# Kernel optimization log

Measured on AMD Instinct MI355X. Metric: run time of the kernel, lower is better.

The kernel has to match this reference:

```python
import jax, jax.numpy as jnp
import numpy as np

# Bit-slice configuration from the module defaults: slices [1,1,2,4] -> 8-bit signed INT.
# The crossbar engine's MapReduceDot decomposes the quantized integers into bit-planes,
# runs partial dot products per (input-slice, weight-slice) pair across paral_size
# partitions, and recombines them with 2^shift weights. In the ideal (noise-free)
# engine this recombination is EXACT, so the forward math equals:
#   dequant(blockwise_quant(x)) @ dequant(blockwise_quant(W^T)) + bias
# with per-block scales determined by the quant granularities.
IN_BITS = 1 + 1 + 2 + 4   # sum(input_slice)  = 8
W_BITS = 1 + 1 + 2 + 4    # sum(weight_slice) = 8
IN_GRAN = (1, 32)         # (rows, cols) blocks over (seq, in_features)
W_GRAN = (32, 32)         # blocks over (in_features, out_features) of weight.t()


def block_fake_quant(x, bits, gran):
    """Symmetric per-block fake quantization (quantize -> dequantize).

    x: [..., R, C]; gran=(gr, gc) tiles the last two dims. Each (gr, gc) block
    gets its own max-abs scale, matching SlicedData's quant_gran semantics.
    """
    qmax = float(2 ** (bits - 1) - 1)  # 127 for 8-bit
    gr, gc = gran
    lead = x.shape[:-2]
    R, C = x.shape[-2], x.shape[-1]
    xb = x.reshape(*lead, R // gr, gr, C // gc, gc)
    mx = jnp.max(jnp.abs(xb), axis=(-3, -1), keepdims=True)
    scale = jnp.where(mx > 0, mx / qmax, jnp.ones_like(mx))
    q = jnp.clip(jnp.round(xb / scale), -qmax, qmax) * scale
    return q.reshape(x.shape)


def setup_inputs() -> dict:
    key = jax.random.key(0)
    k1, k2, k3 = jax.random.split(key, 3)
    B, S, Din, Dout = 4, 4096, 2048, 2048
    x = jax.random.normal(k1, (B, S, Din), dtype=jnp.float32)
    # kaiming_uniform_(a=sqrt(5)) on a Linear weight is U(-1/sqrt(fan_in), 1/sqrt(fan_in))
    bound = 1.0 / np.sqrt(Din)
    weight = jax.random.uniform(k2, (Dout, Din), jnp.float32, -bound, bound)
    bias = jax.random.uniform(k3, (Dout,), jnp.float32, -bound, bound)
    return {"x": x, "weight": weight, "bias": bias}


def reference(x, weight, bias):
    # Quantize activations per (1, 32) block and weight.t() per (32, 32) block,
    # then recombine via the (mathematically exact) bit-sliced dot == dense GEMM
    # on the dequantized values.
    qx = block_fake_quant(x, IN_BITS, IN_GRAN)            # [B, S, Din]
    qw = block_fake_quant(weight.T, W_BITS, W_GRAN)       # [Din, Dout]
    out = jnp.einsum('bsd,de->bse', qx, qw) + bias        # [B, S, Dout]
    return out
```

## Files before the change

kernel.cpp:

```cpp
#include <hip/hip_runtime.h>
#include <hip/hip_bf16.h>
#include <stdint.h>

#define M_TOT 16384
#define N_TOT 2048
#define K_TOT 2048
#define NT 32

typedef __attribute__((ext_vector_type(8))) short bf16x8;
typedef __attribute__((ext_vector_type(4))) float f32x4;

__device__ __forceinline__ ushort f32_to_bf16_rne(float f) {
    uint32_t u = __float_as_uint(f);
    uint32_t r = (u + 0x7fffu + ((u >> 16) & 1u)) >> 16;
    return (ushort)r;
}

__device__ __forceinline__ void async_copy16(const void* gptr, void* lptr) {
    __builtin_amdgcn_global_load_lds(
        (const __attribute__((address_space(1))) uint32_t*)gptr,
        (__attribute__((address_space(3))) uint32_t*)lptr,
        16, 0, 0);
}

__global__ void quant_x_kernel(const float* __restrict__ x, ushort* __restrict__ qx) {
    const int tid = blockIdx.x * 256 + threadIdx.x;
    const float4 v = ((const float4*)x)[tid];
    float m = fmaxf(fmaxf(fabsf(v.x), fabsf(v.y)), fmaxf(fabsf(v.z), fabsf(v.w)));
    m = fmaxf(m, __shfl_xor(m, 1));
    m = fmaxf(m, __shfl_xor(m, 2));
    m = fmaxf(m, __shfl_xor(m, 4));
    const float s = (m > 0.f) ? (m / 127.f) : 1.f;
    const float q0 = fminf(fmaxf(rintf(v.x / s), -127.f), 127.f) * s;
    const float q1 = fminf(fmaxf(rintf(v.y / s), -127.f), 127.f) * s;
    const float q2 = fminf(fmaxf(rintf(v.z / s), -127.f), 127.f) * s;
    const float q3 = fminf(fmaxf(rintf(v.w / s), -127.f), 127.f) * s;
    ushort4 r;
    r.x = f32_to_bf16_rne(q0);
    r.y = f32_to_bf16_rne(q1);
    r.z = f32_to_bf16_rne(q2);
    r.w = f32_to_bf16_rne(q3);
    ((ushort4*)qx)[tid] = r;
}

__global__ void quant_w_kernel(const float* __restrict__ w, ushort* __restrict__ qw) {
    const int gtid = blockIdx.x * 256 + threadIdx.x;
    const int wid  = gtid >> 6;
    const int lane = gtid & 63;
    const int tn = wid >> 6;
    const int tk = wid & 63;
    const int row = tn * 32 + (lane >> 1);
    const int col = tk * 32 + ((lane & 1) << 4);
    const float* p = w + (size_t)row * K_TOT + col;
    const float4 v0 = ((const float4*)p)[0];
    const float4 v1 = ((const float4*)p)[1];
    const float4 v2 = ((const float4*)p)[2];
    const float4 v3 = ((const float4*)p)[3];
    float m = 0.f;
#define MAX4(V) m = fmaxf(m, fmaxf(fmaxf(fabsf(V.x), fabsf(V.y)), fmaxf(fabsf(V.z), fabsf(V.w))));
    MAX4(v0) MAX4(v1) MAX4(v2) MAX4(v3)
#undef MAX4
    #pragma unroll
    for (int off = 1; off < 64; off <<= 1) m = fmaxf(m, __shfl_xor(m, off));
    const float s = (m > 0.f) ? (m / 127.f) : 1.f;
    float vv[16] = {v0.x, v0.y, v0.z, v0.w, v1.x, v1.y, v1.z, v1.w,
                    v2.x, v2.y, v2.z, v2.w, v3.x, v3.y, v3.z, v3.w};
    union { ushort us[16]; uint4 q[2]; } o;
    #pragma unroll
    for (int i = 0; i < 16; ++i) {
        const float q = fminf(fmaxf(rintf(vv[i] / s), -127.f), 127.f) * s;
        o.us[i] = f32_to_bf16_rne(q);
    }
    uint4* dst = (uint4*)(qw + (size_t)row * K_TOT + col);
    dst[0] = o.q[0];
    dst[1] = o.q[1];
}

#define LDSA(tb, row, colus) \
    (*(const bf16x8*)&As[tb][row][(colus) ^ (((row) & 7) << 3)])
#define LDSB(slot, row, colus) \
    (*(const bf16x8*)&Bs[slot][row][(colus) ^ (((row) & 7) << 3)])

#define STAGE_A(tb, hh, li, tt)                                                          \
    async_copy16(Agbase + (size_t)((hh) * 128 + (li) * 64) * K_TOT + (size_t)(tt) * 64,  \
                 (char*)&As[0][0][0] + (tb) * 32768 + (hh) * 16384 + (li) * 8192 + (wv << 10));
#define STAGE_B(slot, hh, li, tt)                                                        \
    async_copy16(Bgbase + (size_t)((hh) * 128 + (li) * 64) * K_TOT + (size_t)(tt) * 64,  \
                 (char*)&Bs[0][0][0] + (size_t)(slot) * 32768 + (hh) * 16384 + (li) * 8192 + (wv << 10));
#define STAGE_A2(tb, hh, tt)    { STAGE_A(tb, hh, 0, tt) STAGE_A(tb, hh, 1, tt) }
#define STAGE_B2(slot, hh, tt)  { STAGE_B(slot, hh, 0, tt) STAGE_B(slot, hh, 1, tt) }

#define WAITLGKM4 { asm volatile("s_waitcnt lgkmcnt(4)" ::: "memory"); __builtin_amdgcn_sched_barrier(0); }
#define WAITLGKM0 { asm volatile("s_waitcnt lgkmcnt(0)" ::: "memory"); __builtin_amdgcn_sched_barrier(0); }

#define RD_AF(DST, tb, q) {                                   \
    DST[0] = LDSA(tb, ab + (q) * 32,      h8);                \
    DST[1] = LDSA(tb, ab + (q) * 32,      32 + h8);           \
    DST[2] = LDSA(tb, ab + (q) * 32 + 16, h8);                \
    DST[3] = LDSA(tb, ab + (q) * 32 + 16, 32 + h8); }

#define RD_BG(slot) {                                                         \
    _Pragma("unroll")                                                         \
    for (int j = 0; j < 4; ++j) {                                             \
        const int bb = wcn * 64 + j * 16 + r;                                 \
        bg[j][0] = LDSB(slot, bb, h8);  bg[j][1] = LDSB(slot, bb, 32 + h8);   \
    } }

#define MFMA_PH(i0, AF)                                                                   \
    __builtin_amdgcn_s_setprio(1);                                                        \
    _Pragma("unroll")                                                                     \
    for (int j = 0; j < 4; ++j) {                                                         \
        acc[i0][j]     = __builtin_amdgcn_mfma_f32_16x16x32_bf16(AF[0], bg[j][0], acc[i0][j], 0, 0, 0);     \
        acc[i0][j]     = __builtin_amdgcn_mfma_f32_16x16x32_bf16(AF[1], bg[j][1], acc[i0][j], 0, 0, 0);     \
        acc[(i0)+1][j] = __builtin_amdgcn_mfma_f32_16x16x32_bf16(AF[2], bg[j][0], acc[(i0)+1][j], 0, 0, 0); \
        acc[(i0)+1][j] = __builtin_amdgcn_mfma_f32_16x16x32_bf16(AF[3], bg[j][1], acc[(i0)+1][j], 0, 0, 0); \
    }                                                                                     \
    __builtin_amdgcn_s_setprio(0);

#define TILE_BODY(tb, t, STA, STB, VMC, BRD, BWR)                                         \
  {                                                                                       \
                   \
    RD_AF(afX, tb, 0)                                                                     \
    RD_BG(BRD)                                                                            \
    RD_AF(afY, tb, 1)                                                                     \
    if (STA) STAGE_A2(tb ^ 1, 0, (t) + 1)                                                 \
    WAITLGKM4                                                                             \
    MFMA_PH(0, afX)                                                                       \
                                        \
    RD_AF(afX, tb, 2)                                                                     \
    if (STA) STAGE_A2(tb ^ 1, 1, (t) + 1)                                                 \
    WAITLGKM4                                                                             \
    MFMA_PH(2, afY)                                                                       \
                     \
    RD_AF(afY, tb, 3)                                                                     \
    if (STB) STAGE_B2(BWR, 0, (t) + 2)                                                    \
    WAITLGKM4                                                                             \
    MFMA_PH(4, afX)                                                                       \
                    \
    if (STB) STAGE_B2(BWR, 1, (t) + 2)                                                    \
    WAITLGKM0                                                                             \
    MFMA_PH(6, afY)                                                                       \
    if ((VMC) == 4)      { asm volatile("s_waitcnt vmcnt(4)" ::: "memory"); }             \
    else if ((VMC) == 0) { asm volatile("s_waitcnt vmcnt(0)" ::: "memory"); }             \
    __builtin_amdgcn_s_barrier();          \
  }

__global__ __launch_bounds__(512, 2) void gemm_pipe5_kernel(
    const ushort* __restrict__ A,
    const ushort* __restrict__ Bt,
    const float* __restrict__ bias,
    float* __restrict__ C) {

    __shared__ ushort As[2][256][64];
    __shared__ ushort Bs[3][256][64];

    const int tid  = threadIdx.x;
    const int lane = tid & 63;
    const int wv   = tid >> 6;
    const int wmr  = wv >> 2;
    const int wcn  = wv & 3;
    const int r    = lane & 15;
    const int h8   = (lane >> 4) << 3;

    const int nbn  = N_TOT / 256;
    const int nwg  = (M_TOT / 256) * nbn;
    const int cpx  = nwg >> 3;
    const int swz  = (blockIdx.x & 7) * cpx + (blockIdx.x >> 3);
    const int brow = (swz / nbn) * 256;
    const int bcol = (swz % nbn) * 256;

    const int srow = tid >> 3;
    const int scol = (((tid & 7) ^ (srow & 7)) << 3);
    const ushort* Agbase = A  + (size_t)(brow + srow) * K_TOT + scol;
    const ushort* Bgbase = Bt + (size_t)(bcol + srow) * K_TOT + scol;

    const int ab = wmr * 128 + r;

    f32x4 acc[8][4];
    const f32x4 zero = {0.f, 0.f, 0.f, 0.f};
    #pragma unroll
    for (int i = 0; i < 8; ++i)
        #pragma unroll
        for (int j = 0; j < 4; ++j) acc[i][j] = zero;

    STAGE_A2(0, 0, 0) STAGE_A2(0, 1, 0)
    STAGE_B2(0, 0, 0) STAGE_B2(0, 1, 0)
    STAGE_B2(1, 0, 1) STAGE_B2(1, 1, 1)
    asm volatile("s_waitcnt vmcnt(4)" ::: "memory");
    __builtin_amdgcn_s_barrier();

    bf16x8 afX[4], afY[4];
    bf16x8 bg[4][2];

    int brd = 0;
    int bwr = 2;

    for (int t = 0; t < NT - 2; t += 2) {
        TILE_BODY(0, t,     1, 1, 4, brd, bwr)
        brd = (brd == 2) ? 0 : brd + 1;  bwr = (bwr == 2) ? 0 : bwr + 1;
        TILE_BODY(1, t + 1, 1, 1, 4, brd, bwr)
        brd = (brd == 2) ? 0 : brd + 1;  bwr = (bwr == 2) ? 0 : bwr + 1;
    }
    TILE_BODY(0, NT - 2, 1, 0, 0, brd, 0)
    brd = (brd == 2) ? 0 : brd + 1;
    TILE_BODY(1, NT - 1, 0, 0, -1, brd, 0)

    const int hq = (lane >> 4) * 4;
    float bv[4];
    #pragma unroll
    for (int j = 0; j < 4; ++j) bv[j] = bias[bcol + wcn * 64 + j * 16 + r];
    #pragma unroll
    for (int i = 0; i < 8; ++i) {
        const int row0 = brow + wmr * 128 + i * 16 + hq;
        #pragma unroll
        for (int j = 0; j < 4; ++j) {
            const int col = bcol + wcn * 64 + j * 16 + r;
            #pragma unroll
            for (int jj = 0; jj < 4; ++jj)
                C[(size_t)(row0 + jj) * N_TOT + col] = acc[i][j][jj] + bv[j];
        }
    }
}

extern "C" void kernel_launch(void* const* d_in, const int* in_sizes, int n_in,
                              void* d_out, int out_size, void* d_ws, size_t ws_size,
                              hipStream_t stream) {
    const float* x    = (const float*)d_in[0];
    const float* wgt  = (const float*)d_in[1];
    const float* bias = (const float*)d_in[2];
    float* out = (float*)d_out;

    ushort* qx = (ushort*)d_ws;
    ushort* qw = qx + (size_t)M_TOT * K_TOT;

    quant_x_kernel<<<(M_TOT * K_TOT / 4) / 256, 256, 0, stream>>>(x, qx);
    quant_w_kernel<<<(64 * 64 * 64) / 256, 256, 0, stream>>>(wgt, qw);
    gemm_pipe5_kernel<<<(M_TOT / 256) * (N_TOT / 256), 512, 0, stream>>>(qx, qw, bias, out);
}
```

Before: 165.3 us.

## Double-buffer B fragments in registers and deepen B global prefetch by one tile

Replaces the single B-fragment register set with two sets (bgA/bgB), so the next tile's B fragments are read from LDS in pieces interleaved with the current tile's MFMA phases. B global staging now runs three tiles ahead instead of two, and a mid-tile barrier is added so the B slot can be safely overwritten. The lgkmcnt waits are retuned per phase. This is meant to hide LDS read latency for B, at the cost of more VGPRs, an extra barrier per tile, and delicate wait-count correctness.

```diff
diff --git a/kernel.cpp b/kernel.cpp
--- a/kernel.cpp
+++ b/kernel.cpp
@@ -90,8 +90,7 @@
 #define STAGE_A2(tb, hh, tt)    { STAGE_A(tb, hh, 0, tt) STAGE_A(tb, hh, 1, tt) }
 #define STAGE_B2(slot, hh, tt)  { STAGE_B(slot, hh, 0, tt) STAGE_B(slot, hh, 1, tt) }
 
-#define WAITLGKM4 { asm volatile("s_waitcnt lgkmcnt(4)" ::: "memory"); __builtin_amdgcn_sched_barrier(0); }
-#define WAITLGKM0 { asm volatile("s_waitcnt lgkmcnt(0)" ::: "memory"); __builtin_amdgcn_sched_barrier(0); }
+#define WAITLG(N) { asm volatile("s_waitcnt lgkmcnt(" #N ")" ::: "memory"); __builtin_amdgcn_sched_barrier(0); }
 
 #define RD_AF(DST, tb, q) {                                   \
     DST[0] = LDSA(tb, ab + (q) * 32,      h8);                \
@@ -99,53 +98,57 @@
     DST[2] = LDSA(tb, ab + (q) * 32 + 16, h8);                \
     DST[3] = LDSA(tb, ab + (q) * 32 + 16, 32 + h8); }
 
-#define RD_BG(slot) {                                                         \
-    _Pragma("unroll")                                                         \
-    for (int j = 0; j < 4; ++j) {                                             \
-        const int bb = wcn * 64 + j * 16 + r;                                 \
-        bg[j][0] = LDSB(slot, bb, h8);  bg[j][1] = LDSB(slot, bb, 32 + h8);   \
-    } }
-
-#define MFMA_PH(i0, AF)                                                                   \
+#define RD_BG2(DST, slot, j) {                                                \
+    const int bb_ = wcn * 64 + (j) * 16 + r;                                  \
+    DST[j][0] = LDSB(slot, bb_, h8);  DST[j][1] = LDSB(slot, bb_, 32 + h8); }
+
+#define MFMA_PH(i0, AF, BGC)                                                              \
     __builtin_amdgcn_s_setprio(1);                                                        \
     _Pragma("unroll")                                                                     \
     for (int j = 0; j < 4; ++j) {                                                         \
-        acc[i0][j]     = __builtin_amdgcn_mfma_f32_16x16x32_bf16(AF[0], bg[j][0], acc[i0][j], 0, 0, 0);     \
-        acc[i0][j]     = __builtin_amdgcn_mfma_f32_16x16x32_bf16(AF[1], bg[j][1], acc[i0][j], 0, 0, 0);     \
-        acc[(i0)+1][j] = __builtin_amdgcn_mfma_f32_16x16x32_bf16(AF[2], bg[j][0], acc[(i0)+1][j], 0, 0, 0); \
-        acc[(i0)+1][j] = __builtin_amdgcn_mfma_f32_16x16x32_bf16(AF[3], bg[j][1], acc[(i0)+1][j], 0, 0, 0); \
+        acc[i0][j]     = __builtin_amdgcn_mfma_f32_16x16x32_bf16(AF[0], BGC[j][0], acc[i0][j], 0, 0, 0);     \
+        acc[i0][j]     = __builtin_amdgcn_mfma_f32_16x16x32_bf16(AF[1], BGC[j][1], acc[i0][j], 0, 0, 0);     \
+        acc[(i0)+1][j] = __builtin_amdgcn_mfma_f32_16x16x32_bf16(AF[2], BGC[j][0], acc[(i0)+1][j], 0, 0, 0); \
+        acc[(i0)+1][j] = __builtin_amdgcn_mfma_f32_16x16x32_bf16(AF[3], BGC[j][1], acc[(i0)+1][j], 0, 0, 0); \
     }                                                                                     \
     __builtin_amdgcn_s_setprio(0);
 
-#define TILE_BODY(tb, t, STA, STB, VMC, BRD, BWR)                                         \
+#define TILE_BODY(tb, t, BGC, BGN, STA, STB, RDBG, VMC, L0, L1, L2, L3)                   \
   {                                                                                       \
-                   \
+                                                                            \
     RD_AF(afX, tb, 0)                                                                     \
-    RD_BG(BRD)                                                                            \
+    __builtin_amdgcn_sched_barrier(0);           \
     RD_AF(afY, tb, 1)                                                                     \
+    if (RDBG) RD_BG2(BGN, brd, 0)                                                         \
     if (STA) STAGE_A2(tb ^ 1, 0, (t) + 1)                                                 \
-    WAITLGKM4                                                                             \
-    MFMA_PH(0, afX)                                                                       \
-                                        \
+    WAITLG(L0)                                                                            \
+    MFMA_PH(0, afX, BGC)                                                                  \
+                                                                            \
     RD_AF(afX, tb, 2)                                                                     \
+    if (RDBG) RD_BG2(BGN, brd, 1)                                                         \
     if (STA) STAGE_A2(tb ^ 1, 1, (t) + 1)                                                 \
-    WAITLGKM4                                                                             \
-    MFMA_PH(2, afY)                                                                       \
-                     \
+    WAITLG(L1)                                                                            \
+    MFMA_PH(2, afY, BGC)                                                                  \
+    __builtin_amdgcn_s_barrier();      \
+                                                                            \
     RD_AF(afY, tb, 3)                                                                     \
-    if (STB) STAGE_B2(BWR, 0, (t) + 2)                                                    \
-    WAITLGKM4                                                                             \
-    MFMA_PH(4, afX)                                                                       \
-                    \
-    if (STB) STAGE_B2(BWR, 1, (t) + 2)                                                    \
-    WAITLGKM0                                                                             \
-    MFMA_PH(6, afY)                                                                       \
+    if (RDBG) RD_BG2(BGN, brd, 2)                                                         \
+    if (STB) STAGE_B2(bwr, 0, (t) + 3)                                                    \
+    WAITLG(L2)                                                                            \
+    MFMA_PH(4, afX, BGC)                                                                  \
+                                                                            \
+    if (RDBG) RD_BG2(BGN, brd, 3)                                                         \
+    if (STB) STAGE_B2(bwr, 1, (t) + 3)                                                    \
+    WAITLG(L3)                                                                            \
+    MFMA_PH(6, afY, BGC)                                                                  \
     if ((VMC) == 4)      { asm volatile("s_waitcnt vmcnt(4)" ::: "memory"); }             \
     else if ((VMC) == 0) { asm volatile("s_waitcnt vmcnt(0)" ::: "memory"); }             \
-    __builtin_amdgcn_s_barrier();          \
+    __builtin_amdgcn_s_barrier();                  \
   }
 
-__global__ __launch_bounds__(512, 2) void gemm_pipe5_kernel(
+#define ROT { brd = (brd == 2) ? 0 : brd + 1;  bwr = (bwr == 2) ? 0 : bwr + 1; }
+
+__global__ __launch_bounds__(512, 2) void gemm_pipe6_kernel(
     const ushort* __restrict__ A,
     const ushort* __restrict__ Bt,
     const float* __restrict__ bias,
@@ -186,24 +189,31 @@
     STAGE_A2(0, 0, 0) STAGE_A2(0, 1, 0)
     STAGE_B2(0, 0, 0) STAGE_B2(0, 1, 0)
     STAGE_B2(1, 0, 1) STAGE_B2(1, 1, 1)
+    STAGE_B2(2, 0, 2) STAGE_B2(2, 1, 2)
     asm volatile("s_waitcnt vmcnt(4)" ::: "memory");
     __builtin_amdgcn_s_barrier();
 
     bf16x8 afX[4], afY[4];
-    bf16x8 bg[4][2];
-
-    int brd = 0;
-    int bwr = 2;
-
-    for (int t = 0; t < NT - 2; t += 2) {
-        TILE_BODY(0, t,     1, 1, 4, brd, bwr)
-        brd = (brd == 2) ? 0 : brd + 1;  bwr = (bwr == 2) ? 0 : bwr + 1;
-        TILE_BODY(1, t + 1, 1, 1, 4, brd, bwr)
-        brd = (brd == 2) ? 0 : brd + 1;  bwr = (bwr == 2) ? 0 : bwr + 1;
+    bf16x8 bgA[4][2], bgB[4][2];
+    RD_BG2(bgA, 0, 0) RD_BG2(bgA, 0, 1) RD_BG2(bgA, 0, 2) RD_BG2(bgA, 0, 3)
+    __builtin_amdgcn_sched_barrier(0);
+
+    int brd = 1;
+    int bwr = 0;
+
+    for (int t = 0; t < 28; t += 2) {
+        TILE_BODY(0, t,     bgA, bgB, 1, 1, 1, 4, 6, 6, 6, 2)
+        ROT
+        TILE_BODY(1, t + 1, bgB, bgA, 1, 1, 1, 4, 6, 6, 6, 2)
+        ROT
     }
-    TILE_BODY(0, NT - 2, 1, 0, 0, brd, 0)
-    brd = (brd == 2) ? 0 : brd + 1;
-    TILE_BODY(1, NT - 1, 0, 0, -1, brd, 0)
+    TILE_BODY(0, 28, bgA, bgB, 1, 1, 1, 4, 6, 6, 6, 2)
+    ROT
+    TILE_BODY(1, 29, bgB, bgA, 1, 0, 1, 0, 6, 6, 6, 2)
+    ROT
+    TILE_BODY(0, 30, bgA, bgB, 1, 0, 1, 0, 6, 6, 6, 2)
+    ROT
+    TILE_BODY(1, 31, bgB, bgA, 0, 0, 0, -1, 4, 4, 4, 0)
 
     const int hq = (lane >> 4) * 4;
     float bv[4];
@@ -235,5 +245,5 @@
 
     quant_x_kernel<<<(M_TOT * K_TOT / 4) / 256, 256, 0, stream>>>(x, qx);
     quant_w_kernel<<<(64 * 64 * 64) / 256, 256, 0, stream>>>(wgt, qw);
-    gemm_pipe5_kernel<<<(M_TOT / 256) * (N_TOT / 256), 512, 0, stream>>>(qx, qw, bias, out);
-}
+    gemm_pipe6_kernel<<<(M_TOT / 256) * (N_TOT / 256), 512, 0, stream>>>(qx, qw, bias, out);
+}
```

Result: slower. 179.8 us (+8.8%).

## Shrink GEMM workgroup tile to 128x128 with four waves

Applied to the files above, without the earlier changes.

Reshapes the GEMM from a 256x256 tile with 8 waves to a 128x128 tile with 4 waves, each wave computing 64x64. Staging, LDS buffers, fragment reads and the MFMA phases are reorganized to fit the smaller tile. The aim is more workgroups and more resident blocks per CU, hiding latency through thread-level parallelism. The cost is lower data reuse per tile, so each element is loaded more often from global and L2, and LDS reads rise per MFMA.

```diff
diff --git a/kernel.cpp b/kernel.cpp
--- a/kernel.cpp
+++ b/kernel.cpp
@@ -81,115 +81,112 @@
 #define LDSB(slot, row, colus) \
     (*(const bf16x8*)&Bs[slot][row][(colus) ^ (((row) & 7) << 3)])
 
-#define STAGE_A(tb, hh, li, tt)                                                          \
-    async_copy16(Agbase + (size_t)((hh) * 128 + (li) * 64) * K_TOT + (size_t)(tt) * 64,  \
-                 (char*)&As[0][0][0] + (tb) * 32768 + (hh) * 16384 + (li) * 8192 + (wv << 10));
-#define STAGE_B(slot, hh, li, tt)                                                        \
-    async_copy16(Bgbase + (size_t)((hh) * 128 + (li) * 64) * K_TOT + (size_t)(tt) * 64,  \
-                 (char*)&Bs[0][0][0] + (size_t)(slot) * 32768 + (hh) * 16384 + (li) * 8192 + (wv << 10));
-#define STAGE_A2(tb, hh, tt)    { STAGE_A(tb, hh, 0, tt) STAGE_A(tb, hh, 1, tt) }
-#define STAGE_B2(slot, hh, tt)  { STAGE_B(slot, hh, 0, tt) STAGE_B(slot, hh, 1, tt) }
-
-#define WAITLGKM4 { asm volatile("s_waitcnt lgkmcnt(4)" ::: "memory"); __builtin_amdgcn_sched_barrier(0); }
-#define WAITLGKM0 { asm volatile("s_waitcnt lgkmcnt(0)" ::: "memory"); __builtin_amdgcn_sched_barrier(0); }
-
-#define RD_AF(DST, tb, q) {                                   \
-    DST[0] = LDSA(tb, ab + (q) * 32,      h8);                \
-    DST[1] = LDSA(tb, ab + (q) * 32,      32 + h8);           \
-    DST[2] = LDSA(tb, ab + (q) * 32 + 16, h8);                \
-    DST[3] = LDSA(tb, ab + (q) * 32 + 16, 32 + h8); }
+#define STAGE_A(tb, q4, tt)                                                              \
+    async_copy16(Agbase + (size_t)((q4) * 32) * K_TOT + (size_t)(tt) * 64,               \
+                 (char*)&As[0][0][0] + (tb) * 16384 + (q4) * 4096 + (wv << 10));
+#define STAGE_B(slot, q4, tt)                                                            \
+    async_copy16(Bgbase + (size_t)((q4) * 32) * K_TOT + (size_t)(tt) * 64,               \
+                 (char*)&Bs[0][0][0] + (size_t)(slot) * 16384 + (q4) * 4096 + (wv << 10));
+
+#define WAITLG(N) { asm volatile("s_waitcnt lgkmcnt(" #N ")" ::: "memory"); __builtin_amdgcn_sched_barrier(0); }
+
+#define RD_AFG(DST, tb, mg) {                                 \
+    DST[0] = LDSA(tb, ab + (mg) * 16,      h8);               \
+    DST[1] = LDSA(tb, ab + (mg) * 16, 32 + h8); }
 
 #define RD_BG(slot) {                                                         \
     _Pragma("unroll")                                                         \
     for (int j = 0; j < 4; ++j) {                                             \
-        const int bb = wcn * 64 + j * 16 + r;                                 \
-        bg[j][0] = LDSB(slot, bb, h8);  bg[j][1] = LDSB(slot, bb, 32 + h8);   \
+        const int bb_ = bbs + j * 16;                                         \
+        bg[j][0] = LDSB(slot, bb_, h8);  bg[j][1] = LDSB(slot, bb_, 32 + h8); \
     } }
 
-#define MFMA_PH(i0, AF)                                                                   \
+#define MFMA_PH(mg, AF)                                                                   \
     __builtin_amdgcn_s_setprio(1);                                                        \
     _Pragma("unroll")                                                                     \
     for (int j = 0; j < 4; ++j) {                                                         \
-        acc[i0][j]     = __builtin_amdgcn_mfma_f32_16x16x32_bf16(AF[0], bg[j][0], acc[i0][j], 0, 0, 0);     \
-        acc[i0][j]     = __builtin_amdgcn_mfma_f32_16x16x32_bf16(AF[1], bg[j][1], acc[i0][j], 0, 0, 0);     \
-        acc[(i0)+1][j] = __builtin_amdgcn_mfma_f32_16x16x32_bf16(AF[2], bg[j][0], acc[(i0)+1][j], 0, 0, 0); \
-        acc[(i0)+1][j] = __builtin_amdgcn_mfma_f32_16x16x32_bf16(AF[3], bg[j][1], acc[(i0)+1][j], 0, 0, 0); \
+        acc[mg][j] = __builtin_amdgcn_mfma_f32_16x16x32_bf16(AF[0], bg[j][0], acc[mg][j], 0, 0, 0); \
+        acc[mg][j] = __builtin_amdgcn_mfma_f32_16x16x32_bf16(AF[1], bg[j][1], acc[mg][j], 0, 0, 0); \
     }                                                                                     \
     __builtin_amdgcn_s_setprio(0);
 
 #define TILE_BODY(tb, t, STA, STB, VMC, BRD, BWR)                                         \
   {                                                                                       \
-                   \
-    RD_AF(afX, tb, 0)                                                                     \
+             \
+    RD_AFG(afX, tb, 0)                                                                    \
     RD_BG(BRD)                                                                            \
-    RD_AF(afY, tb, 1)                                                                     \
-    if (STA) STAGE_A2(tb ^ 1, 0, (t) + 1)                                                 \
-    WAITLGKM4                                                                             \
+    __builtin_amdgcn_sched_barrier(0);           \
+    RD_AFG(afY, tb, 1)                                                                    \
+    if (STA) { STAGE_A(tb ^ 1, 0, (t) + 1) STAGE_A(tb ^ 1, 1, (t) + 1) }                  \
+    WAITLG(2)                                                                             \
     MFMA_PH(0, afX)                                                                       \
-                                        \
-    RD_AF(afX, tb, 2)                                                                     \
-    if (STA) STAGE_A2(tb ^ 1, 1, (t) + 1)                                                 \
-    WAITLGKM4                                                                             \
-    MFMA_PH(2, afY)                                                                       \
-                     \
-    RD_AF(afY, tb, 3)                                                                     \
-    if (STB) STAGE_B2(BWR, 0, (t) + 2)                                                    \
-    WAITLGKM4                                                                             \
-    MFMA_PH(4, afX)                                                                       \
-                    \
-    if (STB) STAGE_B2(BWR, 1, (t) + 2)                                                    \
-    WAITLGKM0                                                                             \
-    MFMA_PH(6, afY)                                                                       \
+                                   \
+    RD_AFG(afX, tb, 2)                                                                    \
+    if (STA) { STAGE_A(tb ^ 1, 2, (t) + 1) STAGE_A(tb ^ 1, 3, (t) + 1) }                  \
+    WAITLG(2)                                                                             \
+    MFMA_PH(1, afY)                                                                       \
+                \
+    RD_AFG(afY, tb, 3)                                                                    \
+    if (STB) { STAGE_B(BWR, 0, (t) + 2) STAGE_B(BWR, 1, (t) + 2) }                        \
+    WAITLG(2)                                                                             \
+    MFMA_PH(2, afX)                                                                       \
+                \
+    if (STB) { STAGE_B(BWR, 2, (t) + 2) STAGE_B(BWR, 3, (t) + 2) }                        \
+    WAITLG(0)                                                                             \
+    MFMA_PH(3, afY)                                                                       \
     if ((VMC) == 4)      { asm volatile("s_waitcnt vmcnt(4)" ::: "memory"); }             \
     else if ((VMC) == 0) { asm volatile("s_waitcnt vmcnt(0)" ::: "memory"); }             \
     __builtin_amdgcn_s_barrier();          \
   }
 
-__global__ __launch_bounds__(512, 2) void gemm_pipe5_kernel(
+#define ROT { brd = (brd == 2) ? 0 : brd + 1;  bwr = (bwr == 2) ? 0 : bwr + 1; }
+
+__global__ __launch_bounds__(256, 2) void gemm_tlp_kernel(
     const ushort* __restrict__ A,
     const ushort* __restrict__ Bt,
     const float* __restrict__ bias,
     float* __restrict__ C) {
 
-    __shared__ ushort As[2][256][64];
-    __shared__ ushort Bs[3][256][64];
+    __shared__ ushort As[2][128][64];
+    __shared__ ushort Bs[3][128][64];
 
     const int tid  = threadIdx.x;
     const int lane = tid & 63;
     const int wv   = tid >> 6;
-    const int wmr  = wv >> 2;
-    const int wcn  = wv & 3;
+    const int wmr  = wv >> 1;
+    const int wcn  = wv & 1;
     const int r    = lane & 15;
     const int h8   = (lane >> 4) << 3;
 
-    const int nbn  = N_TOT / 256;
-    const int nwg  = (M_TOT / 256) * nbn;
+    const int nbn  = N_TOT / 128;
+    const int nwg  = (M_TOT / 128) * nbn;
     const int cpx  = nwg >> 3;
     const int swz  = (blockIdx.x & 7) * cpx + (blockIdx.x >> 3);
-    const int brow = (swz / nbn) * 256;
-    const int bcol = (swz % nbn) * 256;
+    const int brow = (swz / nbn) * 128;
+    const int bcol = (swz % nbn) * 128;
 
     const int srow = tid >> 3;
     const int scol = (((tid & 7) ^ (srow & 7)) << 3);
     const ushort* Agbase = A  + (size_t)(brow + srow) * K_TOT + scol;
     const ushort* Bgbase = Bt + (size_t)(bcol + srow) * K_TOT + scol;
 
-    const int ab = wmr * 128 + r;
-
-    f32x4 acc[8][4];
+    const int ab  = wmr * 64 + r;
+    const int bbs = wcn * 64 + r;
+
+    f32x4 acc[4][4];
     const f32x4 zero = {0.f, 0.f, 0.f, 0.f};
     #pragma unroll
-    for (int i = 0; i < 8; ++i)
+    for (int i = 0; i < 4; ++i)
         #pragma unroll
         for (int j = 0; j < 4; ++j) acc[i][j] = zero;
 
-    STAGE_A2(0, 0, 0) STAGE_A2(0, 1, 0)
-    STAGE_B2(0, 0, 0) STAGE_B2(0, 1, 0)
-    STAGE_B2(1, 0, 1) STAGE_B2(1, 1, 1)
+    STAGE_A(0, 0, 0) STAGE_A(0, 1, 0) STAGE_A(0, 2, 0) STAGE_A(0, 3, 0)
+    STAGE_B(0, 0, 0) STAGE_B(0, 1, 0) STAGE_B(0, 2, 0) STAGE_B(0, 3, 0)
+    STAGE_B(1, 0, 1) STAGE_B(1, 1, 1) STAGE_B(1, 2, 1) STAGE_B(1, 3, 1)
     asm volatile("s_waitcnt vmcnt(4)" ::: "memory");
     __builtin_amdgcn_s_barrier();
 
-    bf16x8 afX[4], afY[4];
+    bf16x8 afX[2], afY[2];
     bf16x8 bg[4][2];
 
     int brd = 0;
@@ -197,9 +194,9 @@
 
     for (int t = 0; t < NT - 2; t += 2) {
         TILE_BODY(0, t,     1, 1, 4, brd, bwr)
-        brd = (brd == 2) ? 0 : brd + 1;  bwr = (bwr == 2) ? 0 : bwr + 1;
+        ROT
         TILE_BODY(1, t + 1, 1, 1, 4, brd, bwr)
-        brd = (brd == 2) ? 0 : brd + 1;  bwr = (bwr == 2) ? 0 : bwr + 1;
+        ROT
     }
     TILE_BODY(0, NT - 2, 1, 0, 0, brd, 0)
     brd = (brd == 2) ? 0 : brd + 1;
@@ -210,8 +207,8 @@
     #pragma unroll
     for (int j = 0; j < 4; ++j) bv[j] = bias[bcol + wcn * 64 + j * 16 + r];
     #pragma unroll
-    for (int i = 0; i < 8; ++i) {
-        const int row0 = brow + wmr * 128 + i * 16 + hq;
+    for (int i = 0; i < 4; ++i) {
+        const int row0 = brow + wmr * 64 + i * 16 + hq;
         #pragma unroll
         for (int j = 0; j < 4; ++j) {
             const int col = bcol + wcn * 64 + j * 16 + r;
@@ -235,5 +232,5 @@
 
     quant_x_kernel<<<(M_TOT * K_TOT / 4) / 256, 256, 0, stream>>>(x, qx);
     quant_w_kernel<<<(64 * 64 * 64) / 256, 256, 0, stream>>>(wgt, qw);
-    gemm_pipe5_kernel<<<(M_TOT / 256) * (N_TOT / 256), 512, 0, stream>>>(qx, qw, bias, out);
-}
+    gemm_tlp_kernel<<<(M_TOT / 128) * (N_TOT / 128), 256, 0, stream>>>(qx, qw, bias, out);
+}
```

Measured after the change: 191.3 us. +15.7%, slower.
